# Optimization experiments

Hardware: AMD Instinct MI355X
Metric: run time of the kernel (lower is better)

The kernel has to match this reference:

```python
import jax, jax.numpy as jnp
import numpy as np

N = 50000
E = 800000
C_IN, C_HID, C_OUT = 512, 128, 2
HEADS2 = 3
NEG_SLOPE = 0.2


def gat_conv(x, src, dst, W, att_src, att_dst, bias, heads, ch, concat):
    """PyG GATConv (eval mode) on pre-augmented (self-loop included) edge lists.
    x: [N, F_in], W: [F_in, heads*ch], att_*: [heads, ch], bias: [heads*ch] or [ch].
    """
    n = x.shape[0]
    h = (x @ W).reshape(n, heads, ch)                 # [N, H, C]
    a_src = (h * att_src).sum(-1)                     # [N, H]
    a_dst = (h * att_dst).sum(-1)                     # [N, H]
    e = jax.nn.leaky_relu(a_src[src] + a_dst[dst], NEG_SLOPE)  # [E', H]
    # segment softmax over edges sharing a destination node
    m = jax.ops.segment_max(e, dst, num_segments=n)
    m = jnp.where(jnp.isfinite(m), m, 0.0)
    ex = jnp.exp(e - m[dst])
    denom = jax.ops.segment_sum(ex, dst, num_segments=n)
    alpha = ex / (denom[dst] + 1e-16)                 # [E', H]
    out = jax.ops.segment_sum(h[src] * alpha[:, :, None], dst, num_segments=n)  # [N, H, C]
    out = out.reshape(n, heads * ch) if concat else out.mean(axis=1)
    return out + bias


def setup_inputs() -> dict:
    key = jax.random.key(0)
    ks = jax.random.split(key, 12)
    x = jax.random.normal(ks[0], (N, C_IN), dtype=jnp.float32)
    edge_index = jax.random.randint(ks[1], (2, E), 0, N, dtype=jnp.int64)
    s1 = 1.0 / np.sqrt(C_IN)
    s2 = 1.0 / np.sqrt(C_HID)
    return {
        "x": x,
        "edge_index": edge_index,
        "W1": jax.random.normal(ks[2], (C_IN, C_HID), dtype=jnp.float32) * s1,
        "att_src1": jax.random.normal(ks[3], (1, C_HID), dtype=jnp.float32) * s2,
        "att_dst1": jax.random.normal(ks[4], (1, C_HID), dtype=jnp.float32) * s2,
        "bias1": jnp.zeros((C_HID,), dtype=jnp.float32),
        "W2": jax.random.normal(ks[5], (C_HID, HEADS2 * C_OUT), dtype=jnp.float32) * s2,
        "att_src2": jax.random.normal(ks[6], (HEADS2, C_OUT), dtype=jnp.float32) * 0.5,
        "att_dst2": jax.random.normal(ks[7], (HEADS2, C_OUT), dtype=jnp.float32) * 0.5,
        "bias2": jnp.zeros((C_OUT,), dtype=jnp.float32),
    }


def reference(x, edge_index, W1, att_src1, att_dst1, bias1, W2, att_src2, att_dst2, bias2):
    n = x.shape[0]
    loop = jnp.arange(n, dtype=edge_index.dtype)
    src = jnp.concatenate([edge_index[0], loop])      # PyG add_self_loops=True
    dst = jnp.concatenate([edge_index[1], loop])
    h = gat_conv(x, src, dst, W1, att_src1, att_dst1, bias1, 1, C_HID, True)
    h = jax.nn.relu(h)                                # Dropout is identity in eval
    out = gat_conv(h, src, dst, W2, att_src2, att_dst2, bias2, HEADS2, C_OUT, False)
    return out
```

## Files before the change

kernel.cpp:

```cpp
#include <hip/hip_runtime.h>

#define N_NODES 50000
#define N_EDGES 800000
#define E_TOT   850000
#define C_IN    512
#define C_HID   128
#define NEG     0.2f

typedef _Float16 f16x8 __attribute__((ext_vector_type(8)));
typedef __attribute__((ext_vector_type(4))) float f32x4;

__device__ __forceinline__ float leaky(float x) { return x > 0.f ? x : NEG * x; }

union U32H2 { unsigned u; _Float16 h[2]; float f; };
union BFrag { uint4 u; f16x8 h; };

__device__ __forceinline__ unsigned short f2h(float f) {
  U32H2 c; c.h[0] = (_Float16)f; return (unsigned short)(c.u & 0xffff);
}

__device__ __forceinline__ unsigned pk2h(float a, float b) {
  union { __fp16 v __attribute__((ext_vector_type(2))); unsigned u; } c;
  c.v = __builtin_amdgcn_cvt_pkrtz(a, b);
  return c.u;
}

__global__ __launch_bounds__(256) void prep_v_kernel(const float* __restrict__ W1,
    const float* __restrict__ as1, const float* __restrict__ ad1,
    float* __restrict__ v1s, float* __restrict__ v1d) {
  const int wv = threadIdx.x >> 6, lane = threadIdx.x & 63;
  const int k = blockIdx.x * 4 + wv;
  if (k >= C_IN) return;
  float2 w = *(const float2*)(W1 + (size_t)k * C_HID + 2 * lane);
  float2 a = *(const float2*)(as1 + 2 * lane);
  float2 d = *(const float2*)(ad1 + 2 * lane);
  float s = w.x * a.x + w.y * a.y;
  float t = w.x * d.x + w.y * d.y;
#pragma unroll
  for (int m = 32; m >= 1; m >>= 1) {
    s += __shfl_xor(s, m, 64);
    t += __shfl_xor(t, m, 64);
  }
  if (lane == 0) { v1s[k] = s; v1d[k] = t; }
}

__global__ __launch_bounds__(256) void prep_w_kernel(const float* __restrict__ W1,
    unsigned short* __restrict__ Wswz) {
  int t = blockIdx.x * 256 + threadIdx.x;
  int c = t >> 6, kc = t & 63;
  if (c >= C_HID) return;
  int kblk = kc >> 2, q = kc & 3;
  int ct = c >> 4, l15 = c & 15;
  int lane = q * 16 + l15;
  unsigned short hb[8], lb[8];
#pragma unroll
  for (int i = 0; i < 8; i++) {
    float w = W1[(size_t)(kc * 8 + i) * C_HID + c];
    _Float16 hi = (_Float16)w;
    _Float16 lo = (_Float16)(w - (float)hi);
    U32H2 ch; ch.h[0] = hi;
    U32H2 cl; cl.h[0] = lo;
    hb[i] = (unsigned short)(ch.u & 0xffff);
    lb[i] = (unsigned short)(cl.u & 0xffff);
  }
  size_t chunk0 = ((size_t)(kblk * 8 + ct) * 2) * 512;
  *(uint4*)&Wswz[chunk0 + (size_t)lane * 8]       = *(uint4*)hb;
  *(uint4*)&Wswz[chunk0 + 512 + (size_t)lane * 8] = *(uint4*)lb;
}

__global__ __launch_bounds__(256) void lin1_kernel(const float* __restrict__ x,
    const unsigned short* __restrict__ Wswz,
    const float* __restrict__ v1s, const float* __restrict__ v1d,
    unsigned short* __restrict__ h1u, float* __restrict__ a_src, float* __restrict__ a_dst) {
  __shared__ __attribute__((aligned(16))) unsigned short As[64][40];

  const int tid  = threadIdx.x;
  const int lane = tid & 63, wv = tid >> 6;
  const int m0   = blockIdx.x * 64;

  const int arow = tid >> 2, kseg = (tid & 3) * 8;
  int grow = m0 + arow;
  if (grow >= N_NODES) grow = N_NODES - 1;
  const float* xrow = x + (size_t)grow * C_IN + kseg;

  f32x4 acc[4][2];
#pragma unroll
  for (int rt = 0; rt < 4; rt++) { acc[rt][0] = (f32x4)0.f; acc[rt][1] = (f32x4)0.f; }
  float ps = 0.f, pd = 0.f;

  const int q = lane >> 4, l15 = lane & 15;

  float4 xa = *(const float4*)(xrow);
  float4 xb = *(const float4*)(xrow + 4);

  for (int kblk = 0; kblk < 16; kblk++) {
    const int k0 = kblk * 32;
    float4 vsa = *(const float4*)(v1s + k0 + kseg);
    float4 vsb = *(const float4*)(v1s + k0 + kseg + 4);
    float4 vda = *(const float4*)(v1d + k0 + kseg);
    float4 vdb = *(const float4*)(v1d + k0 + kseg + 4);
    ps += xa.x * vsa.x + xa.y * vsa.y + xa.z * vsa.z + xa.w * vsa.w
        + xb.x * vsb.x + xb.y * vsb.y + xb.z * vsb.z + xb.w * vsb.w;
    pd += xa.x * vda.x + xa.y * vda.y + xa.z * vda.z + xa.w * vda.w
        + xb.x * vdb.x + xb.y * vdb.y + xb.z * vdb.z + xb.w * vdb.w;
    uint4 pk = make_uint4(pk2h(xa.x, xa.y), pk2h(xa.z, xa.w),
                          pk2h(xb.x, xb.y), pk2h(xb.z, xb.w));

    __syncthreads();
    *(uint4*)&As[arow][kseg] = pk;
    if (kblk < 15) {
      xa = *(const float4*)(xrow + k0 + 32);
      xb = *(const float4*)(xrow + k0 + 36);
    }
    __syncthreads();

    const unsigned short* bp = Wswz + ((size_t)(kblk * 8 + wv * 2) * 2) * 512 + (size_t)lane * 8;
    BFrag b00, b01, b10, b11;
    b00.u = *(const uint4*)(bp);
    b01.u = *(const uint4*)(bp + 512);
    b10.u = *(const uint4*)(bp + 1024);
    b11.u = *(const uint4*)(bp + 1536);

#pragma unroll
    for (int rt = 0; rt < 4; rt++) {
      f16x8 af = *(const f16x8*)&As[rt * 16 + l15][q * 8];
      acc[rt][0] = __builtin_amdgcn_mfma_f32_16x16x32_f16(af, b00.h, acc[rt][0], 0, 0, 0);
      acc[rt][0] = __builtin_amdgcn_mfma_f32_16x16x32_f16(af, b01.h, acc[rt][0], 0, 0, 0);
      acc[rt][1] = __builtin_amdgcn_mfma_f32_16x16x32_f16(af, b10.h, acc[rt][1], 0, 0, 0);
      acc[rt][1] = __builtin_amdgcn_mfma_f32_16x16x32_f16(af, b11.h, acc[rt][1], 0, 0, 0);
    }
  }

  ps += __shfl_xor(ps, 1, 64); ps += __shfl_xor(ps, 2, 64);
  pd += __shfl_xor(pd, 1, 64); pd += __shfl_xor(pd, 2, 64);
  if ((tid & 3) == 0) {
    int row = m0 + arow;
    if (row < N_NODES) { a_src[row] = ps; a_dst[row] = pd; }
  }

#pragma unroll
  for (int rt = 0; rt < 4; rt++) {
    int rbase = m0 + rt * 16 + q * 4;
#pragma unroll
    for (int ct = 0; ct < 2; ct++) {
      int col = wv * 32 + ct * 16 + l15;
#pragma unroll
      for (int ri = 0; ri < 4; ri++) {
        int row = rbase + ri;
        if (row < N_NODES)
          h1u[(size_t)row * C_HID + col] = f2h(acc[rt][ct][ri]);
      }
    }
  }
}

__global__ void deg_kernel(const int* __restrict__ ei, int* __restrict__ deg) {
  int e = blockIdx.x * blockDim.x + threadIdx.x;
  if (e >= N_EDGES) return;
  atomicAdd(&deg[ei[N_EDGES + e]], 1);
}

__global__ __launch_bounds__(1024) void scan_kernel(const int* __restrict__ deg,
                                                    int* __restrict__ rowptr,
                                                    int* __restrict__ cursor) {
  __shared__ int wsum[16];
  const int tid = threadIdx.x, lane = tid & 63, wv = tid >> 6;
  int carry = 0;
  for (int base = 0; base < N_NODES; base += 8192) {
    int i0 = base + tid * 8;
    int v[8];
    if (i0 + 8 <= N_NODES) {
      int4 va = *(const int4*)(deg + i0);
      int4 vb = *(const int4*)(deg + i0 + 4);
      v[0]=va.x+1; v[1]=va.y+1; v[2]=va.z+1; v[3]=va.w+1;
      v[4]=vb.x+1; v[5]=vb.y+1; v[6]=vb.z+1; v[7]=vb.w+1;
    } else {
#pragma unroll
      for (int i = 0; i < 8; i++) v[i] = (i0 + i < N_NODES) ? deg[i0 + i] + 1 : 0;
    }
    int tsum = 0;
#pragma unroll
    for (int i = 0; i < 8; i++) tsum += v[i];
    int sc = tsum;
#pragma unroll
    for (int off = 1; off < 64; off <<= 1) {
      int t = __shfl_up(sc, off, 64);
      if (lane >= off) sc += t;
    }
    if (lane == 63) wsum[wv] = sc;
    __syncthreads();
    if (wv == 0 && lane < 16) {
      int s = wsum[lane];
#pragma unroll
      for (int off = 1; off < 16; off <<= 1) {
        int t = __shfl_up(s, off, 64);
        if (lane >= off) s += t;
      }
      wsum[lane] = s;
    }
    __syncthreads();
    int ex = carry + (wv ? wsum[wv - 1] : 0) + sc - tsum;
#pragma unroll
    for (int i = 0; i < 8; i++) {
      if (i0 + i < N_NODES) { rowptr[i0 + i] = ex; cursor[i0 + i] = ex; }
      ex += v[i];
    }
    carry += wsum[15];
    __syncthreads();
  }
  if (tid == 0) rowptr[N_NODES] = carry;
}

__global__ void bucket_kernel(const int* __restrict__ ei, int* __restrict__ cursor,
                              const float* __restrict__ a_src, const float* __restrict__ a_dst,
                              int2* __restrict__ esw) {
  int e = blockIdx.x * blockDim.x + threadIdx.x;
  if (e >= E_TOT) return;
  int src, dst;
  if (e < N_EDGES) { src = ei[e]; dst = ei[N_EDGES + e]; }
  else             { src = dst = e - N_EDGES; }
  float w = __expf(leaky(a_src[src] + a_dst[dst]));
  int slot = atomicAdd(&cursor[dst], 1);
  U32H2 c; c.f = w;
  esw[slot] = make_int2(src, (int)c.u);
}

__global__ __launch_bounds__(256) void agg1_kernel(const unsigned short* __restrict__ h1u,
    const int2* __restrict__ esw, const int* __restrict__ rowptr,
    const float* __restrict__ bias1, const float* __restrict__ W2,
    const float* __restrict__ as2w, const float* __restrict__ ad2w,
    float* __restrict__ h2, float* __restrict__ as2, float* __restrict__ ad2) {
  const int wv = threadIdx.x >> 6, lane = threadIdx.x & 63;
  const int q = lane >> 4, r = lane & 15;
  const int n = blockIdx.x * 4 + wv;
  if (n >= N_NODES) return;
  const int start = rowptr[n], end = rowptr[n + 1];

  float acc[8];
#pragma unroll
  for (int i = 0; i < 8; i++) acc[i] = 0.f;
  float wsum = 0.f;

  const unsigned short* hbase = h1u + r * 8;

  for (int base = start; base < end; base += 64) {
    int idx = base + lane;
    int sreg = 0; float wreg = 0.f;
    if (idx < end) {
      int2 sv = esw[idx];
      sreg = sv.x;
      U32H2 c; c.u = (unsigned)sv.y;
      wreg = c.f;
    }
    wsum += wreg;
    const int cnt = min(64, end - base);
    const int nit = (cnt + 7) >> 3;
    for (int i = 0; i < nit; i++) {
      int e0 = 8 * i + q, e1 = 8 * i + 4 + q;
      int   s0 = __shfl(sreg, e0, 64);
      int   s1 = __shfl(sreg, e1, 64);
      float w0 = __shfl(wreg, e0, 64);
      float w1 = __shfl(wreg, e1, 64);
      uint4 g0 = *(const uint4*)(hbase + (size_t)s0 * C_HID);
      uint4 g1 = *(const uint4*)(hbase + (size_t)s1 * C_HID);
      U32H2 c0, c1, c2, c3;
      c0.u = g0.x; c1.u = g0.y; c2.u = g0.z; c3.u = g0.w;
      acc[0] = fmaf(w0, (float)c0.h[0], acc[0]); acc[1] = fmaf(w0, (float)c0.h[1], acc[1]);
      acc[2] = fmaf(w0, (float)c1.h[0], acc[2]); acc[3] = fmaf(w0, (float)c1.h[1], acc[3]);
      acc[4] = fmaf(w0, (float)c2.h[0], acc[4]); acc[5] = fmaf(w0, (float)c2.h[1], acc[5]);
      acc[6] = fmaf(w0, (float)c3.h[0], acc[6]); acc[7] = fmaf(w0, (float)c3.h[1], acc[7]);
      c0.u = g1.x; c1.u = g1.y; c2.u = g1.z; c3.u = g1.w;
      acc[0] = fmaf(w1, (float)c0.h[0], acc[0]); acc[1] = fmaf(w1, (float)c0.h[1], acc[1]);
      acc[2] = fmaf(w1, (float)c1.h[0], acc[2]); acc[3] = fmaf(w1, (float)c1.h[1], acc[3]);
      acc[4] = fmaf(w1, (float)c2.h[0], acc[4]); acc[5] = fmaf(w1, (float)c2.h[1], acc[5]);
      acc[6] = fmaf(w1, (float)c3.h[0], acc[6]); acc[7] = fmaf(w1, (float)c3.h[1], acc[7]);
    }
  }

#pragma unroll
  for (int i = 0; i < 8; i++) {
    acc[i] += __shfl_xor(acc[i], 16, 64);
    acc[i] += __shfl_xor(acc[i], 32, 64);
  }
#pragma unroll
  for (int m = 32; m >= 1; m >>= 1) wsum += __shfl_xor(wsum, m, 64);
  const float inv = 1.f / wsum;

  float4 ba = *(const float4*)(bias1 + r * 8);
  float4 bb = *(const float4*)(bias1 + r * 8 + 4);
  float u[8] = {fmaxf(acc[0] * inv + ba.x, 0.f), fmaxf(acc[1] * inv + ba.y, 0.f),
                fmaxf(acc[2] * inv + ba.z, 0.f), fmaxf(acc[3] * inv + ba.w, 0.f),
                fmaxf(acc[4] * inv + bb.x, 0.f), fmaxf(acc[5] * inv + bb.y, 0.f),
                fmaxf(acc[6] * inv + bb.z, 0.f), fmaxf(acc[7] * inv + bb.w, 0.f)};
  float p[6] = {0, 0, 0, 0, 0, 0};
#pragma unroll
  for (int i = 0; i < 8; i++) {
    const float* w2r = W2 + (size_t)(r * 8 + i) * 6;
#pragma unroll
    for (int o = 0; o < 6; o++) p[o] = fmaf(u[i], w2r[o], p[o]);
  }
#pragma unroll
  for (int o = 0; o < 6; o++) {
#pragma unroll
    for (int msk = 8; msk >= 1; msk >>= 1) p[o] += __shfl_xor(p[o], msk, 64);
  }

  if (lane == 0) {
#pragma unroll
    for (int o = 0; o < 6; o++) h2[(size_t)n * 8 + o] = p[o];
#pragma unroll
    for (int h = 0; h < 3; h++) {
      as2[n * 4 + h] = p[2 * h] * as2w[2 * h] + p[2 * h + 1] * as2w[2 * h + 1];
      ad2[n * 4 + h] = p[2 * h] * ad2w[2 * h] + p[2 * h + 1] * ad2w[2 * h + 1];
    }
  }
}

__global__ __launch_bounds__(256) void agg2_kernel(const float* __restrict__ h2,
    const float* __restrict__ as2, const float* __restrict__ ad2,
    const int* __restrict__ rowptr, const int2* __restrict__ esw,
    const float* __restrict__ bias2, float* __restrict__ out) {
  const int wv = threadIdx.x >> 6, lane = threadIdx.x & 63;
  const int q = lane >> 4, r = lane & 15;
  const int n = blockIdx.x * 16 + wv * 4 + q;
  if (n >= N_NODES) return;
  const int start = rowptr[n], end = rowptr[n + 1];
  const float4 adv = *(const float4*)(ad2 + (size_t)n * 4);

  float d0 = 0.f, d1 = 0.f, d2 = 0.f;
  float a0 = 0.f, a1 = 0.f, a2 = 0.f, a3 = 0.f, a4 = 0.f, a5 = 0.f;
  for (int j = start + r; j < end; j += 16) {
    int s = esw[j].x;
    float4 asv = *(const float4*)(as2 + (size_t)s * 4);
    float4 hlo = *(const float4*)(h2 + (size_t)s * 8);
    float2 hhi = *(const float2*)(h2 + (size_t)s * 8 + 4);
    float e0 = __expf(leaky(asv.x + adv.x));
    float e1 = __expf(leaky(asv.y + adv.y));
    float e2 = __expf(leaky(asv.z + adv.z));
    d0 += e0; d1 += e1; d2 += e2;
    a0 += e0 * hlo.x; a1 += e0 * hlo.y;
    a2 += e1 * hlo.z; a3 += e1 * hlo.w;
    a4 += e2 * hhi.x; a5 += e2 * hhi.y;
  }
#pragma unroll
  for (int m = 8; m >= 1; m >>= 1) {
    d0 += __shfl_xor(d0, m, 64); d1 += __shfl_xor(d1, m, 64); d2 += __shfl_xor(d2, m, 64);
    a0 += __shfl_xor(a0, m, 64); a1 += __shfl_xor(a1, m, 64); a2 += __shfl_xor(a2, m, 64);
    a3 += __shfl_xor(a3, m, 64); a4 += __shfl_xor(a4, m, 64); a5 += __shfl_xor(a5, m, 64);
  }
  if (r == 0) {
    float o0 = (a0 / d0 + a2 / d1 + a4 / d2) * (1.f / 3.f) + bias2[0];
    float o1 = (a1 / d0 + a3 / d1 + a5 / d2) * (1.f / 3.f) + bias2[1];
    *(float2*)(out + (size_t)n * 2) = make_float2(o0, o1);
  }
}

extern "C" void kernel_launch(void* const* d_in, const int* in_sizes, int n_in,
                              void* d_out, int out_size, void* d_ws, size_t ws_size,
                              hipStream_t stream) {
  const float* x        = (const float*)d_in[0];
  const int*   ei       = (const int*)d_in[1];
  const float* W1       = (const float*)d_in[2];
  const float* att_src1 = (const float*)d_in[3];
  const float* att_dst1 = (const float*)d_in[4];
  const float* bias1    = (const float*)d_in[5];
  const float* W2       = (const float*)d_in[6];
  const float* att_src2 = (const float*)d_in[7];
  const float* att_dst2 = (const float*)d_in[8];
  const float* bias2    = (const float*)d_in[9];
  float* out = (float*)d_out;

  char* w = (char*)d_ws;
  auto alloc = [&](size_t bytes) {
    char* p = w;
    w += (bytes + 255) & ~(size_t)255;
    return p;
  };
  unsigned short* h1u    = (unsigned short*)alloc((size_t)N_NODES * C_HID * 2);
  unsigned short* Wswz   = (unsigned short*)alloc((size_t)C_IN * C_HID * 2 * 2);
  float*          v1s    = (float*)alloc((size_t)C_IN * 4);
  float*          v1d    = (float*)alloc((size_t)C_IN * 4);
  float*          a_src1 = (float*)alloc((size_t)N_NODES * 4);
  float*          a_dst1 = (float*)alloc((size_t)N_NODES * 4);
  int*            deg    = (int*)alloc((size_t)N_NODES * 4);
  int*            rowptr = (int*)alloc((size_t)(N_NODES + 4) * 4);
  int*            cursor = (int*)alloc((size_t)N_NODES * 4);
  int2*           esw    = (int2*)alloc((size_t)E_TOT * 8);
  float*          h2     = (float*)alloc((size_t)N_NODES * 8 * 4);
  float*          as2    = (float*)alloc((size_t)N_NODES * 4 * 4);
  float*          ad2    = (float*)alloc((size_t)N_NODES * 4 * 4);

  (void)hipMemsetAsync(deg, 0, (size_t)N_NODES * 4, stream);

  prep_v_kernel<<<C_IN / 4, 256, 0, stream>>>(W1, att_src1, att_dst1, v1s, v1d);
  prep_w_kernel<<<32, 256, 0, stream>>>(W1, Wswz);
  deg_kernel<<<(N_EDGES + 255) / 256, 256, 0, stream>>>(ei, deg);
  scan_kernel<<<1, 1024, 0, stream>>>(deg, rowptr, cursor);
  lin1_kernel<<<(N_NODES + 63) / 64, 256, 0, stream>>>(x, Wswz, v1s, v1d,
                                                       h1u, a_src1, a_dst1);
  bucket_kernel<<<(E_TOT + 255) / 256, 256, 0, stream>>>(ei, cursor, a_src1, a_dst1, esw);
  agg1_kernel<<<(N_NODES + 3) / 4, 256, 0, stream>>>(h1u, esw, rowptr, bias1, W2,
                                                     att_src2, att_dst2, h2, as2, ad2);
  agg2_kernel<<<(N_NODES + 15) / 16, 256, 0, stream>>>(h2, as2, ad2, rowptr, esw, bias2, out);
}
```

Measured before the change: 354.1 us.

## Split h1 into column groups and aggregate each group in a separate block

lin1 now writes h1 as four column-group planes of 32 fp16 channels each, so each plane is a contiguous N x 32 table. agg1 launches four blocks per node group, each gathering only 4-byte slices from one plane, which shrinks the gathered working set per pass so it fits better in cache. The partial layer-2 projections are combined with atomicAdds into h2/as2/ad2, which now need a memset first. Edge records are also written and read with nontemporal hints. The trade-offs are that the edge list is read four times and that atomics and extra index shuffles are added.

New measurement: 448.0 us. 26.5% more time.

```diff
diff --git a/kernel.cpp b/kernel.cpp
--- a/kernel.cpp
+++ b/kernel.cpp
@@ -71,7 +71,7 @@
 __global__ __launch_bounds__(256) void lin1_kernel(const float* __restrict__ x,
     const unsigned short* __restrict__ Wswz,
     const float* __restrict__ v1s, const float* __restrict__ v1d,
-    unsigned short* __restrict__ h1u, float* __restrict__ a_src, float* __restrict__ a_dst) {
+    unsigned short* __restrict__ h1g, float* __restrict__ a_src, float* __restrict__ a_dst) {
   __shared__ __attribute__((aligned(16))) unsigned short As[64][40];
 
   const int tid  = threadIdx.x;
@@ -143,12 +143,12 @@
     int rbase = m0 + rt * 16 + q * 4;
 #pragma unroll
     for (int ct = 0; ct < 2; ct++) {
-      int col = wv * 32 + ct * 16 + l15;
 #pragma unroll
       for (int ri = 0; ri < 4; ri++) {
         int row = rbase + ri;
         if (row < N_NODES)
-          h1u[(size_t)row * C_HID + col] = f2h(acc[rt][ct][ri]);
+          h1g[(size_t)wv * N_NODES * 32 + (size_t)row * 32 + ct * 16 + l15]
+              = f2h(acc[rt][ct][ri]);
       }
     }
   }
@@ -222,83 +222,66 @@
   float w = __expf(leaky(a_src[src] + a_dst[dst]));
   int slot = atomicAdd(&cursor[dst], 1);
   U32H2 c; c.f = w;
-  esw[slot] = make_int2(src, (int)c.u);
-}
-
-__global__ __launch_bounds__(256) void agg1_kernel(const unsigned short* __restrict__ h1u,
+  unsigned long long pack = (unsigned long long)(unsigned)src
+                          | ((unsigned long long)c.u << 32);
+  __builtin_nontemporal_store(pack, (unsigned long long*)(esw + slot));
+}
+
+__global__ __launch_bounds__(256) void agg1_kernel(const unsigned short* __restrict__ h1g,
     const int2* __restrict__ esw, const int* __restrict__ rowptr,
     const float* __restrict__ bias1, const float* __restrict__ W2,
     const float* __restrict__ as2w, const float* __restrict__ ad2w,
     float* __restrict__ h2, float* __restrict__ as2, float* __restrict__ ad2) {
   const int wv = threadIdx.x >> 6, lane = threadIdx.x & 63;
   const int q = lane >> 4, r = lane & 15;
-  const int n = blockIdx.x * 4 + wv;
-  if (n >= N_NODES) return;
+  const int g = blockIdx.x & 3;
+  const int n = (blockIdx.x >> 2) * 4 + wv;
+
   const int start = rowptr[n], end = rowptr[n + 1];
-
-  float acc[8];
-#pragma unroll
-  for (int i = 0; i < 8; i++) acc[i] = 0.f;
-  float wsum = 0.f;
-
-  const unsigned short* hbase = h1u + r * 8;
-
+  const unsigned short* tbl = h1g + (size_t)g * N_NODES * 32 + r * 2;
+
+  float acc0 = 0.f, acc1 = 0.f, wsum = 0.f;
   for (int base = start; base < end; base += 64) {
     int idx = base + lane;
     int sreg = 0; float wreg = 0.f;
     if (idx < end) {
-      int2 sv = esw[idx];
-      sreg = sv.x;
-      U32H2 c; c.u = (unsigned)sv.y;
+      unsigned long long v =
+          __builtin_nontemporal_load((const unsigned long long*)(esw + idx));
+      sreg = (int)(unsigned)(v & 0xffffffffull);
+      U32H2 c; c.u = (unsigned)(v >> 32);
       wreg = c.f;
     }
     wsum += wreg;
     const int cnt = min(64, end - base);
-    const int nit = (cnt + 7) >> 3;
-    for (int i = 0; i < nit; i++) {
-      int e0 = 8 * i + q, e1 = 8 * i + 4 + q;
-      int   s0 = __shfl(sreg, e0, 64);
-      int   s1 = __shfl(sreg, e1, 64);
-      float w0 = __shfl(wreg, e0, 64);
-      float w1 = __shfl(wreg, e1, 64);
-      uint4 g0 = *(const uint4*)(hbase + (size_t)s0 * C_HID);
-      uint4 g1 = *(const uint4*)(hbase + (size_t)s1 * C_HID);
-      U32H2 c0, c1, c2, c3;
-      c0.u = g0.x; c1.u = g0.y; c2.u = g0.z; c3.u = g0.w;
-      acc[0] = fmaf(w0, (float)c0.h[0], acc[0]); acc[1] = fmaf(w0, (float)c0.h[1], acc[1]);
-      acc[2] = fmaf(w0, (float)c1.h[0], acc[2]); acc[3] = fmaf(w0, (float)c1.h[1], acc[3]);
-      acc[4] = fmaf(w0, (float)c2.h[0], acc[4]); acc[5] = fmaf(w0, (float)c2.h[1], acc[5]);
-      acc[6] = fmaf(w0, (float)c3.h[0], acc[6]); acc[7] = fmaf(w0, (float)c3.h[1], acc[7]);
-      c0.u = g1.x; c1.u = g1.y; c2.u = g1.z; c3.u = g1.w;
-      acc[0] = fmaf(w1, (float)c0.h[0], acc[0]); acc[1] = fmaf(w1, (float)c0.h[1], acc[1]);
-      acc[2] = fmaf(w1, (float)c1.h[0], acc[2]); acc[3] = fmaf(w1, (float)c1.h[1], acc[3]);
-      acc[4] = fmaf(w1, (float)c2.h[0], acc[4]); acc[5] = fmaf(w1, (float)c2.h[1], acc[5]);
-      acc[6] = fmaf(w1, (float)c3.h[0], acc[6]); acc[7] = fmaf(w1, (float)c3.h[1], acc[7]);
-    }
-  }
-
-#pragma unroll
-  for (int i = 0; i < 8; i++) {
-    acc[i] += __shfl_xor(acc[i], 16, 64);
-    acc[i] += __shfl_xor(acc[i], 32, 64);
-  }
+#pragma unroll
+    for (int blk = 0; blk < 2; blk++) {
+      if (blk * 32 >= cnt) break;
+#pragma unroll
+      for (int i = 0; i < 8; i++) {
+        int slot = blk * 32 + i * 4 + q;
+        int   s = __shfl(sreg, slot, 64);
+        float w = __shfl(wreg, slot, 64);
+        U32H2 cv; cv.u = *(const unsigned*)(tbl + (size_t)s * 32);
+        acc0 = fmaf(w, (float)cv.h[0], acc0);
+        acc1 = fmaf(w, (float)cv.h[1], acc1);
+      }
+    }
+  }
+
+  acc0 += __shfl_xor(acc0, 16, 64); acc0 += __shfl_xor(acc0, 32, 64);
+  acc1 += __shfl_xor(acc1, 16, 64); acc1 += __shfl_xor(acc1, 32, 64);
 #pragma unroll
   for (int m = 32; m >= 1; m >>= 1) wsum += __shfl_xor(wsum, m, 64);
   const float inv = 1.f / wsum;
 
-  float4 ba = *(const float4*)(bias1 + r * 8);
-  float4 bb = *(const float4*)(bias1 + r * 8 + 4);
-  float u[8] = {fmaxf(acc[0] * inv + ba.x, 0.f), fmaxf(acc[1] * inv + ba.y, 0.f),
-                fmaxf(acc[2] * inv + ba.z, 0.f), fmaxf(acc[3] * inv + ba.w, 0.f),
-                fmaxf(acc[4] * inv + bb.x, 0.f), fmaxf(acc[5] * inv + bb.y, 0.f),
-                fmaxf(acc[6] * inv + bb.z, 0.f), fmaxf(acc[7] * inv + bb.w, 0.f)};
-  float p[6] = {0, 0, 0, 0, 0, 0};
-#pragma unroll
-  for (int i = 0; i < 8; i++) {
-    const float* w2r = W2 + (size_t)(r * 8 + i) * 6;
-#pragma unroll
-    for (int o = 0; o < 6; o++) p[o] = fmaf(u[i], w2r[o], p[o]);
-  }
+  const int c0 = g * 32 + r * 2;
+  float2 b = *(const float2*)(bias1 + c0);
+  float u0 = fmaxf(acc0 * inv + b.x, 0.f);
+  float u1 = fmaxf(acc1 * inv + b.y, 0.f);
+  float p[6];
+  const float* w2a = W2 + (size_t)c0 * 6;
+#pragma unroll
+  for (int o = 0; o < 6; o++) p[o] = u0 * w2a[o] + u1 * w2a[6 + o];
 #pragma unroll
   for (int o = 0; o < 6; o++) {
 #pragma unroll
@@ -307,11 +290,11 @@
 
   if (lane == 0) {
 #pragma unroll
-    for (int o = 0; o < 6; o++) h2[(size_t)n * 8 + o] = p[o];
+    for (int o = 0; o < 6; o++) atomicAdd(&h2[(size_t)n * 8 + o], p[o]);
 #pragma unroll
     for (int h = 0; h < 3; h++) {
-      as2[n * 4 + h] = p[2 * h] * as2w[2 * h] + p[2 * h + 1] * as2w[2 * h + 1];
-      ad2[n * 4 + h] = p[2 * h] * ad2w[2 * h] + p[2 * h + 1] * ad2w[2 * h + 1];
+      atomicAdd(&as2[n * 4 + h], p[2 * h] * as2w[2 * h] + p[2 * h + 1] * as2w[2 * h + 1]);
+      atomicAdd(&ad2[n * 4 + h], p[2 * h] * ad2w[2 * h] + p[2 * h + 1] * ad2w[2 * h + 1]);
     }
   }
 }
@@ -330,7 +313,9 @@
   float d0 = 0.f, d1 = 0.f, d2 = 0.f;
   float a0 = 0.f, a1 = 0.f, a2 = 0.f, a3 = 0.f, a4 = 0.f, a5 = 0.f;
   for (int j = start + r; j < end; j += 16) {
-    int s = esw[j].x;
+    unsigned long long v =
+        __builtin_nontemporal_load((const unsigned long long*)(esw + j));
+    int s = (int)(unsigned)(v & 0xffffffffull);
     float4 asv = *(const float4*)(as2 + (size_t)s * 4);
     float4 hlo = *(const float4*)(h2 + (size_t)s * 8);
     float2 hhi = *(const float2*)(h2 + (size_t)s * 8 + 4);
@@ -376,7 +361,7 @@
     w += (bytes + 255) & ~(size_t)255;
     return p;
   };
-  unsigned short* h1u    = (unsigned short*)alloc((size_t)N_NODES * C_HID * 2);
+  unsigned short* h1g    = (unsigned short*)alloc((size_t)N_NODES * C_HID * 2);
   unsigned short* Wswz   = (unsigned short*)alloc((size_t)C_IN * C_HID * 2 * 2);
   float*          v1s    = (float*)alloc((size_t)C_IN * 4);
   float*          v1d    = (float*)alloc((size_t)C_IN * 4);
@@ -391,15 +376,16 @@
   float*          ad2    = (float*)alloc((size_t)N_NODES * 4 * 4);
 
   (void)hipMemsetAsync(deg, 0, (size_t)N_NODES * 4, stream);
+  (void)hipMemsetAsync(h2, 0, (size_t)N_NODES * (8 + 4 + 4) * 4, stream);
 
   prep_v_kernel<<<C_IN / 4, 256, 0, stream>>>(W1, att_src1, att_dst1, v1s, v1d);
   prep_w_kernel<<<32, 256, 0, stream>>>(W1, Wswz);
   deg_kernel<<<(N_EDGES + 255) / 256, 256, 0, stream>>>(ei, deg);
   scan_kernel<<<1, 1024, 0, stream>>>(deg, rowptr, cursor);
   lin1_kernel<<<(N_NODES + 63) / 64, 256, 0, stream>>>(x, Wswz, v1s, v1d,
-                                                       h1u, a_src1, a_dst1);
+                                                       h1g, a_src1, a_dst1);
   bucket_kernel<<<(E_TOT + 255) / 256, 256, 0, stream>>>(ei, cursor, a_src1, a_dst1, esw);
-  agg1_kernel<<<(N_NODES + 3) / 4, 256, 0, stream>>>(h1u, esw, rowptr, bias1, W2,
+  agg1_kernel<<<(N_NODES / 4) * 4, 256, 0, stream>>>(h1g, esw, rowptr, bias1, W2,
                                                      att_src2, att_dst2, h2, as2, ad2);
   agg2_kernel<<<(N_NODES + 15) / 16, 256, 0, stream>>>(h2, as2, ad2, rowptr, esw, bias2, out);
 }
```
